# Kernel optimization log

Measured on AMD Instinct MI355X. Metric: run time of the kernel, lower is better.

## Reference

```python
import jax, jax.numpy as jnp
import numpy as np

GROUP_SIZE = 128


def setup_inputs() -> dict:
    key = jax.random.key(0)
    k1, k2, k3 = jax.random.split(key, 3)
    B, S, IN, OUT = 4, 8192, 1024, 1024
    x = jax.random.normal(k1, (B, S, IN), dtype=jnp.float32)
    weight = jax.random.normal(k2, (OUT, IN), dtype=jnp.float32) * 0.02
    bias = jax.random.normal(k3, (OUT,), dtype=jnp.float32) * 0.01
    return {"x": x, "weight": weight, "bias": bias}


def reference(x, weight, bias):
    """Quantized int8 path: quantize() + _forward_int8 of OneBitLinear.

    - weights binarized to +/-1 int8 (sign, with 0 -> -1, matching
      sign().clamp(min=0) bit packing then 2*bit-1)
    - per-group weight scales = group absmax, stored fp16 (as in quantize())
    - activations dynamically quantized per-token to int8
    - int32-accumulated GEMM, rescaled by x_scale * mean group scale per row
    """
    out_f, in_f = weight.shape
    ng = in_f // GROUP_SIZE
    w_g = weight.reshape(out_f, ng, GROUP_SIZE)
    # per-group absmax scales, cast fp16 -> fp32 to mimic fp16 storage
    scales = jnp.maximum(jnp.max(jnp.abs(w_g), axis=-1), 1e-8)
    scales = scales.astype(jnp.float16).astype(jnp.float32)  # [O, ng]
    # +/-1 int8 weights (sign>0 -> +1, else -1; zero maps to -1 like the packer)
    w_int8 = jnp.where(weight > 0, 1, -1).astype(jnp.int8)  # [O, I]

    # dynamic per-token activation quantization
    x_f = x.reshape(-1, in_f)  # [BT, I]
    x_scale = jnp.maximum(jnp.max(jnp.abs(x_f), axis=1, keepdims=True), 1e-8) / 127.0
    x_int8 = jnp.clip(jnp.round(x_f / x_scale), -128, 127).astype(jnp.int8)

    # int8 GEMM with int32 accumulation
    out_i32 = jnp.matmul(
        x_int8.astype(jnp.int32), w_int8.T.astype(jnp.int32)
    )  # [BT, O]

    w_scale_per_row = jnp.mean(scales, axis=1)  # [O]
    out_f32 = out_i32.astype(jnp.float32) * x_scale * w_scale_per_row[None, :]
    out_f32 = out_f32 + bias[None, :]
    return out_f32.reshape(*x.shape[:-1], out_f)
```

## Files before the change

### kernel.cpp

```cpp
#include <hip/hip_runtime.h>
#include <hip/hip_fp16.h>

#define K_DIM 1024
#define N_DIM 1024

typedef int v4i __attribute__((ext_vector_type(4)));

__device__ __forceinline__ void async_load16(const void* g, void* l) {
    __builtin_amdgcn_global_load_lds(
        (const __attribute__((address_space(1))) unsigned int*)g,
        (__attribute__((address_space(3))) unsigned int*)l,
        16, 0, 0);
}

__global__ __launch_bounds__(256) void prep_w(const float* __restrict__ w,
                                              signed char* __restrict__ wq,
                                              float* __restrict__ wscale) {
    const int lane = threadIdx.x & 63;
    const int row  = blockIdx.x * 4 + (threadIdx.x >> 6);
    const float4* wr = (const float4*)(w + (size_t)row * K_DIM);
    float4 v[4];
#pragma unroll
    for (int j = 0; j < 4; ++j) v[j] = wr[lane * 4 + j];

    float g = 0.f;
#pragma unroll
    for (int j = 0; j < 4; ++j) {
        g = fmaxf(g, fabsf(v[j].x)); g = fmaxf(g, fabsf(v[j].y));
        g = fmaxf(g, fabsf(v[j].z)); g = fmaxf(g, fabsf(v[j].w));
    }
    g = fmaxf(g, __shfl_xor(g, 1, 64));
    g = fmaxf(g, __shfl_xor(g, 2, 64));
    g = fmaxf(g, __shfl_xor(g, 4, 64));
    const float s = __half2float(__float2half(fmaxf(g, 1e-8f)));
    float t = s;
    t += __shfl_xor(t, 8, 64);
    t += __shfl_xor(t, 16, 64);
    t += __shfl_xor(t, 32, 64);
    if (lane == 0) wscale[row] = t * 0.125f;

    int pk[4];
#pragma unroll
    for (int j = 0; j < 4; ++j) {
        const int b0 = (v[j].x > 0.f) ? 1 : -1;
        const int b1 = (v[j].y > 0.f) ? 1 : -1;
        const int b2 = (v[j].z > 0.f) ? 1 : -1;
        const int b3 = (v[j].w > 0.f) ? 1 : -1;
        pk[j] = (b0 & 255) | ((b1 & 255) << 8) | ((b2 & 255) << 16) | (b3 << 24);
    }
    *(int4*)(wq + (size_t)row * K_DIM + lane * 16) = make_int4(pk[0], pk[1], pk[2], pk[3]);
}

__global__ __launch_bounds__(256) void quant_x(const float* __restrict__ x,
                                               signed char* __restrict__ xq,
                                               float* __restrict__ xs) {
    const int lane = threadIdx.x & 63;
    const int row  = blockIdx.x * 4 + (threadIdx.x >> 6);
    const float4* xr = (const float4*)(x + (size_t)row * K_DIM);
    float4 v[4];
#pragma unroll
    for (int j = 0; j < 4; ++j) v[j] = xr[lane + 64 * j];

    float am = 0.f;
#pragma unroll
    for (int j = 0; j < 4; ++j) {
        am = fmaxf(am, fabsf(v[j].x)); am = fmaxf(am, fabsf(v[j].y));
        am = fmaxf(am, fabsf(v[j].z)); am = fmaxf(am, fabsf(v[j].w));
    }
#pragma unroll
    for (int off = 32; off >= 1; off >>= 1) am = fmaxf(am, __shfl_xor(am, off, 64));
    const float scale = fmaxf(am, 1e-8f) / 127.f;

    int* xqi = (int*)(xq + (size_t)row * K_DIM);
#pragma unroll
    for (int j = 0; j < 4; ++j) {
        const int b0 = (int)fminf(fmaxf(rintf(v[j].x / scale), -128.f), 127.f);
        const int b1 = (int)fminf(fmaxf(rintf(v[j].y / scale), -128.f), 127.f);
        const int b2 = (int)fminf(fmaxf(rintf(v[j].z / scale), -128.f), 127.f);
        const int b3 = (int)fminf(fmaxf(rintf(v[j].w / scale), -128.f), 127.f);
        xqi[lane + 64 * j] = (b0 & 255) | ((b1 & 255) << 8) | ((b2 & 255) << 16) | (b3 << 24);
    }
    if (lane == 0) xs[row] = scale;
}

__global__ __launch_bounds__(256) void gemm_i8(const signed char* __restrict__ A,
                                               const signed char* __restrict__ Bw,
                                               const float* __restrict__ xs,
                                               const float* __restrict__ wscale,
                                               const float* __restrict__ bias,
                                               float* __restrict__ out) {
    __shared__ __align__(16) signed char As[128 * 128];
    __shared__ __align__(16) signed char Bs[128 * 128];

    const int tid  = threadIdx.x;
    const int lane = tid & 63;
    const int wave = tid >> 6;
    const int wm = wave >> 1;
    const int wn = wave & 1;

    const int bid   = blockIdx.x;
    const int nT    = bid & 7;
    const size_t mBase = (size_t)(bid >> 3) * 128;
    const int nBase = nT * 128;

    v4i acc[4][4] = {};

    const int srow = tid >> 3;
    const int scol = (tid & 7) * 16;
    const signed char* Ag = A  + (mBase + srow) * K_DIM + scol;
    const signed char* Bg = Bw + (size_t)(nBase + srow) * K_DIM + scol;

    for (int kt = 0; kt < 8; ++kt) {
        const int koff = kt * 128;
#pragma unroll
        for (int c = 0; c < 4; ++c) {
            async_load16(Ag + (size_t)(c * 32) * K_DIM + koff, As + c * 4096 + tid * 16);
            async_load16(Bg + (size_t)(c * 32) * K_DIM + koff, Bs + c * 4096 + tid * 16);
        }
        __syncthreads();

#pragma unroll
        for (int ks = 0; ks < 2; ++ks) {
            v4i af[4], bf[4];
#pragma unroll
            for (int mt = 0; mt < 4; ++mt)
                af[mt] = *(const v4i*)(As + (wm * 64 + mt * 16 + (lane & 15)) * 128
                                          + ks * 64 + (lane >> 4) * 16);
#pragma unroll
            for (int nt = 0; nt < 4; ++nt)
                bf[nt] = *(const v4i*)(Bs + (wn * 64 + nt * 16 + (lane & 15)) * 128
                                          + ks * 64 + (lane >> 4) * 16);
#pragma unroll
            for (int mt = 0; mt < 4; ++mt)
#pragma unroll
                for (int nt = 0; nt < 4; ++nt)
                    acc[mt][nt] = __builtin_amdgcn_mfma_i32_16x16x64_i8(
                        af[mt], bf[nt], acc[mt][nt], 0, 0, 0);
        }
        __syncthreads();
    }

    const int cc = lane & 15;
    const int rq = (lane >> 4) * 4;
    float xsr[4][4];
#pragma unroll
    for (int mt = 0; mt < 4; ++mt)
#pragma unroll
        for (int i = 0; i < 4; ++i)
            xsr[mt][i] = xs[mBase + wm * 64 + mt * 16 + rq + i];

#pragma unroll
    for (int nt = 0; nt < 4; ++nt) {
        const int col  = nBase + wn * 64 + nt * 16 + cc;
        const float wsc = wscale[col];
        const float bb  = bias[col];
#pragma unroll
        for (int mt = 0; mt < 4; ++mt) {
#pragma unroll
            for (int i = 0; i < 4; ++i) {
                const size_t row = mBase + wm * 64 + mt * 16 + rq + i;
                out[row * N_DIM + col] = ((float)acc[mt][nt][i] * xsr[mt][i]) * wsc + bb;
            }
        }
    }
}

extern "C" void kernel_launch(void* const* d_in, const int* in_sizes, int n_in,
                              void* d_out, int out_size, void* d_ws, size_t ws_size,
                              hipStream_t stream) {
    const float* x    = (const float*)d_in[0];
    const float* w    = (const float*)d_in[1];
    const float* bias = (const float*)d_in[2];
    float* out = (float*)d_out;

    const int BT = in_sizes[0] / K_DIM;

    char* ws = (char*)d_ws;
    signed char* xq     = (signed char*)ws;
    float*       xs     = (float*)(ws + (size_t)BT * K_DIM);
    signed char* wq     = (signed char*)(ws + (size_t)BT * K_DIM + (size_t)BT * 4);
    float*       wscale = (float*)((char*)wq + (size_t)N_DIM * K_DIM);

    prep_w<<<N_DIM / 4, 256, 0, stream>>>(w, wq, wscale);
    quant_x<<<BT / 4, 256, 0, stream>>>(x, xq, xs);
    gemm_i8<<<(BT / 128) * (N_DIM / 128), 256, 0, stream>>>(xq, wq, xs, wscale, bias, out);
}
```

Baseline: 292.2 us.

## Swizzle LDS tiles, remap blocks per XCD, vectorize quant_x stores

The GEMM XORs the 16-byte column chunk with the row index when loading tiles into LDS and reading them back, so the fragment reads no longer hit the same banks. Block IDs are also remapped so that blocks landing on the same XCD share nearby M tiles, which should improve L2 reuse of A across the N tiles. quant_x now loads contiguous float4s per lane, multiplies by a reciprocal instead of dividing, and writes one 16-byte store per lane. The reciprocal multiply can round differently from the reference division in rare cases.

```diff
diff --git a/kernel.cpp b/kernel.cpp
--- a/kernel.cpp
+++ b/kernel.cpp
@@ -59,7 +59,7 @@
     const float4* xr = (const float4*)(x + (size_t)row * K_DIM);
     float4 v[4];
 #pragma unroll
-    for (int j = 0; j < 4; ++j) v[j] = xr[lane + 64 * j];
+    for (int j = 0; j < 4; ++j) v[j] = xr[lane * 4 + j];
 
     float am = 0.f;
 #pragma unroll
@@ -70,16 +70,18 @@
 #pragma unroll
     for (int off = 32; off >= 1; off >>= 1) am = fmaxf(am, __shfl_xor(am, off, 64));
     const float scale = fmaxf(am, 1e-8f) / 127.f;
+    const float inv   = 1.0f / scale;
 
-    int* xqi = (int*)(xq + (size_t)row * K_DIM);
+    int pk[4];
 #pragma unroll
     for (int j = 0; j < 4; ++j) {
-        const int b0 = (int)fminf(fmaxf(rintf(v[j].x / scale), -128.f), 127.f);
-        const int b1 = (int)fminf(fmaxf(rintf(v[j].y / scale), -128.f), 127.f);
-        const int b2 = (int)fminf(fmaxf(rintf(v[j].z / scale), -128.f), 127.f);
-        const int b3 = (int)fminf(fmaxf(rintf(v[j].w / scale), -128.f), 127.f);
-        xqi[lane + 64 * j] = (b0 & 255) | ((b1 & 255) << 8) | ((b2 & 255) << 16) | (b3 << 24);
+        const int b0 = (int)fminf(fmaxf(rintf(v[j].x * inv), -128.f), 127.f);
+        const int b1 = (int)fminf(fmaxf(rintf(v[j].y * inv), -128.f), 127.f);
+        const int b2 = (int)fminf(fmaxf(rintf(v[j].z * inv), -128.f), 127.f);
+        const int b3 = (int)fminf(fmaxf(rintf(v[j].w * inv), -128.f), 127.f);
+        pk[j] = (b0 & 255) | ((b1 & 255) << 8) | ((b2 & 255) << 16) | (b3 << 24);
     }
+    *(int4*)(xq + (size_t)row * K_DIM + lane * 16) = make_int4(pk[0], pk[1], pk[2], pk[3]);
     if (lane == 0) xs[row] = scale;
 }
 
@@ -98,15 +100,18 @@
     const int wm = wave >> 1;
     const int wn = wave & 1;
 
-    const int bid   = blockIdx.x;
-    const int nT    = bid & 7;
-    const size_t mBase = (size_t)(bid >> 3) * 128;
-    const int nBase = nT * 128;
+    const int bid = blockIdx.x;
+    const int xcd = bid & 7;
+    const int q   = bid >> 3;
+    const int mT  = xcd * 32 + (q >> 3);
+    const int nT  = q & 7;
+    const size_t mBase = (size_t)mT * 128;
+    const int    nBase = nT * 128;
 
     v4i acc[4][4] = {};
 
     const int srow = tid >> 3;
-    const int scol = (tid & 7) * 16;
+    const int scol = (((tid & 7) ^ (srow & 7))) * 16;
     const signed char* Ag = A  + (mBase + srow) * K_DIM + scol;
     const signed char* Bg = Bw + (size_t)(nBase + srow) * K_DIM + scol;
 
@@ -119,17 +124,19 @@
         }
         __syncthreads();
 
+        const int r16 = lane & 15;
+        const int g   = lane >> 4;
+        const int x7  = lane & 7;
 #pragma unroll
         for (int ks = 0; ks < 2; ++ks) {
+            const int co = ((ks * 4 + g) ^ x7) * 16;
             v4i af[4], bf[4];
 #pragma unroll
             for (int mt = 0; mt < 4; ++mt)
-                af[mt] = *(const v4i*)(As + (wm * 64 + mt * 16 + (lane & 15)) * 128
-                                          + ks * 64 + (lane >> 4) * 16);
+                af[mt] = *(const v4i*)(As + (wm * 64 + mt * 16 + r16) * 128 + co);
 #pragma unroll
             for (int nt = 0; nt < 4; ++nt)
-                bf[nt] = *(const v4i*)(Bs + (wn * 64 + nt * 16 + (lane & 15)) * 128
-                                          + ks * 64 + (lane >> 4) * 16);
+                bf[nt] = *(const v4i*)(Bs + (wn * 64 + nt * 16 + r16) * 128 + co);
 #pragma unroll
             for (int mt = 0; mt < 4; ++mt)
 #pragma unroll
```

New measurement: 276.6 us. 5.3% less time.
